# Kernel tuning notes

Measured on AMD Instinct MI355X. Metric: run time of the kernel, lower is better.

The kernel has to match this reference:

```python
import jax, jax.numpy as jnp
import numpy as np

B, T, C, H, D = 2, 2048, 1024, 16, 64


def setup_inputs() -> dict:
    key = jax.random.key(0)
    k1, k2, k3, k4, k5 = jax.random.split(key, 5)
    x = jax.random.normal(k1, (B, T, C), dtype=jnp.float32)
    Wq = jax.random.normal(k2, (H, C, D), dtype=jnp.float32) * 0.02
    Wk = jax.random.normal(k3, (H, C, D), dtype=jnp.float32) * 0.02
    Wv = jax.random.normal(k4, (H, C, D), dtype=jnp.float32) * 0.02
    Wo = jax.random.normal(k5, (C, C), dtype=jnp.float32) * 0.02
    bo = jnp.zeros((C,), dtype=jnp.float32)
    return {"x": x, "Wq": Wq, "Wk": Wk, "Wv": Wv, "Wo": Wo, "bo": bo}


def reference(x, Wq, Wk, Wv, Wo, bo):
    # per-head projections (batched over heads instead of a python loop)
    q = jnp.einsum('btc,hcd->bhtd', x, Wq)
    k = jnp.einsum('btc,hcd->bhtd', x, Wk)
    v = jnp.einsum('btc,hcd->bhtd', x, Wv)
    scale = jnp.asarray(D, x.dtype) ** -0.5
    wei = jnp.einsum('bhtd,bhsd->bhts', q, k) * scale  # [B,H,T,T]
    causal = jnp.tril(jnp.ones((T, T), dtype=bool))
    wei = jnp.where(causal, wei, jnp.asarray(-jnp.inf, wei.dtype))
    attn = jax.nn.softmax(wei, axis=-1)
    out = jnp.einsum('bhts,bhsd->bhtd', attn, v)  # [B,H,T,D]
    # concat heads (head order h0..hH-1 along feature dim)
    out = out.transpose(0, 2, 1, 3).reshape(B, T, C)
    # output projection: nn.Linear -> y = x @ W^T + b  (dropout p=0 is identity)
    return out @ Wo.T + bo
```

## Files before the change

### kernel.cpp

```cpp
#include <hip/hip_runtime.h>
#include <hip/hip_bf16.h>
#include <cstdint>
#include <math.h>

#define B_DIM 2
#define T_SEQ 2048
#define C_DIM 1024
#define H_NUM 16
#define D_HEAD 64
#define M_ROWS (B_DIM * T_SEQ)
#define N_QKV (3 * H_NUM * D_HEAD)

using short8  = __attribute__((ext_vector_type(8))) short;
using short4v = __attribute__((ext_vector_type(4))) short;
using f32x4   = __attribute__((ext_vector_type(4))) float;

__device__ __forceinline__ short f2bf(float f) {
  union { __hip_bfloat16 h; short s; } u;
  u.h = __float2bfloat16(f);
  return u.s;
}

__device__ __forceinline__ unsigned pk2bf(float a, float b) {
  union { float f; unsigned u; } ua, ub;
  ua.f = a; ub.f = b;
  return __builtin_amdgcn_perm(ub.u, ua.u, 0x07060302u);
}

__device__ __forceinline__ void gld_lds16(short* lds, const short* g) {
  __builtin_amdgcn_global_load_lds(
      (const unsigned int __attribute__((address_space(1)))*)g,
      (unsigned int __attribute__((address_space(3)))*)lds, 16, 0, 0);
}

#define BAR_VM(N)                                                    \
  do {                                                               \
    asm volatile("s_waitcnt vmcnt(" #N ") lgkmcnt(0)" ::: "memory"); \
    __builtin_amdgcn_s_barrier();                                    \
    __builtin_amdgcn_sched_barrier(0);                               \
  } while (0)

__global__ __launch_bounds__(256) void cvt_f32_bf16(const float* __restrict__ in,
                                                    short* __restrict__ out, int n8) {
  int i = blockIdx.x * 256 + threadIdx.x;
  if (i >= n8) return;
  const float4* p = reinterpret_cast<const float4*>(in) + (size_t)i * 2;
  float4 a = p[0], b = p[1];
  short8 o;
  o[0] = f2bf(a.x); o[1] = f2bf(a.y); o[2] = f2bf(a.z); o[3] = f2bf(a.w);
  o[4] = f2bf(b.x); o[5] = f2bf(b.y); o[6] = f2bf(b.z); o[7] = f2bf(b.w);
  reinterpret_cast<short8*>(out)[i] = o;
}

__global__ __launch_bounds__(256) void pack_w(const float* __restrict__ Wq,
                                              const float* __restrict__ Wk,
                                              const float* __restrict__ Wv,
                                              short* __restrict__ Wt) {
  int bid  = blockIdx.x;
  int proj = bid >> 8;
  int h    = (bid >> 4) & 15;
  int cb   = bid & 15;
  const float* W = (proj == 0) ? Wq : ((proj == 1) ? Wk : Wv);
  const float* src = W + ((size_t)h * C_DIM + (size_t)cb * 64) * D_HEAD;

  __shared__ float tile[64][65];
  int tid = threadIdx.x;

#pragma unroll
  for (int j = 0; j < 4; j++) {
    int flat = tid + j * 256;
    int c    = flat >> 4;
    int d4   = flat & 15;
    float4 v = reinterpret_cast<const float4*>(src + (size_t)c * D_HEAD)[d4];
    tile[c][d4 * 4 + 0] = v.x;
    tile[c][d4 * 4 + 1] = v.y;
    tile[c][d4 * 4 + 2] = v.z;
    tile[c][d4 * 4 + 3] = v.w;
  }
  __syncthreads();

  int d     = tid >> 2;
  int cpart = (tid & 3) * 16;
  short* dst = Wt + ((size_t)(proj * H_NUM + h) * D_HEAD + d) * C_DIM + cb * 64 + cpart;
  short8 o0, o1;
#pragma unroll
  for (int j = 0; j < 8; j++) {
    o0[j] = f2bf(tile[cpart + j][d]);
    o1[j] = f2bf(tile[cpart + 8 + j][d]);
  }
  *reinterpret_cast<short8*>(dst)     = o0;
  *reinterpret_cast<short8*>(dst + 8) = o1;
}

template <int MODE, int BMT>
__global__ __launch_bounds__(256) void gemm_bt(
    const short* __restrict__ A, const short* __restrict__ Bt,
    const float* __restrict__ bias,
    short* __restrict__ qb, short* __restrict__ kb, short* __restrict__ vtb,
    float* __restrict__ outb,
    int M, int N, int K) {
  constexpr int BK = 32;
  constexpr int MR = BMT / 32;
  constexpr int NLA = BMT / 64;
  __shared__ short GL[3 * (BMT + 128) * BK];
  short* Asb = GL;
  short* Bsb = GL + 3 * BMT * BK;

  int tid  = threadIdx.x;
  int lane = tid & 63;
  int wv   = tid >> 6;
  int q15  = lane & 15, g = lane >> 4;
  int ntn  = N >> 7;
  int bpx  = (M / BMT) >> 3;
  int xcd  = blockIdx.x & 7;
  int idx  = blockIdx.x >> 3;
  int bn   = idx / bpx;
  int bm   = xcd * bpx + (idx - bn * bpx);
  int row0 = bm * BMT, col0 = bn << 7;
  int wm   = (wv >> 1) * (BMT / 2);
  int wn   = (wv & 1) << 6;

  f32x4 acc[MR][4];
#pragma unroll
  for (int i = 0; i < MR; i++)
#pragma unroll
    for (int j = 0; j < 4; j++) acc[i][j] = (f32x4){0.f, 0.f, 0.f, 0.f};

  const short* ag = A  + (size_t)(row0 + (tid >> 2)) * K + (tid & 3) * 8;
  const short* bg = Bt + (size_t)(col0 + (tid >> 2)) * K + (tid & 3) * 8;
  const size_t gstep = (size_t)64 * K;

  auto stage = [&](int ks, int buf) {
    const short* a  = ag + (size_t)ks * BK;
    const short* bb = bg + (size_t)ks * BK;
    gld_lds16(Asb + buf * BMT * BK + tid * 8, a);
    if constexpr (NLA == 2)
      gld_lds16(Asb + buf * BMT * BK + 64 * BK + tid * 8, a + gstep);
    gld_lds16(Bsb + buf * 128 * BK + tid * 8, bb);
    gld_lds16(Bsb + buf * 128 * BK + 64 * BK + tid * 8, bb + gstep);
  };

  int nk = K / BK;
  stage(0, 0);
  stage(1, 1);
  if constexpr (NLA == 2) {
    asm volatile("s_waitcnt vmcnt(4)" ::: "memory");
  } else {
    asm volatile("s_waitcnt vmcnt(3)" ::: "memory");
  }
  __builtin_amdgcn_s_barrier();
  __builtin_amdgcn_sched_barrier(0);

  for (int k = 0; k < nk; ++k) {
    int buf = k % 3;
    if (k + 2 < nk) stage(k + 2, (k + 2) % 3);

    short8 af[MR], bf[4];
#pragma unroll
    for (int mi = 0; mi < MR; mi++)
      af[mi] = *reinterpret_cast<const short8*>(
          &Asb[buf * BMT * BK + (wm + mi * 16 + q15) * BK + g * 8]);
#pragma unroll
    for (int ni = 0; ni < 4; ni++)
      bf[ni] = *reinterpret_cast<const short8*>(
          &Bsb[buf * 128 * BK + (wn + ni * 16 + q15) * BK + g * 8]);
    __builtin_amdgcn_s_setprio(1);
#pragma unroll
    for (int mi = 0; mi < MR; mi++)
#pragma unroll
      for (int ni = 0; ni < 4; ni++)
        acc[mi][ni] = __builtin_amdgcn_mfma_f32_16x16x32_bf16(af[mi], bf[ni],
                                                              acc[mi][ni], 0, 0, 0);
    __builtin_amdgcn_s_setprio(0);

    if (k + 1 < nk) {
      if (k + 2 < nk) {
        if constexpr (NLA == 2) { BAR_VM(4); } else { BAR_VM(3); }
      } else {
        BAR_VM(0);
      }
    }
  }

  if constexpr (MODE == 0) {
    constexpr int LDT = 136;
    int proj  = col0 >> 10;
    int b     = row0 >> 11;
    int trow0 = row0 & (T_SEQ - 1);
    int h0    = (col0 >> 6) & 15;
    __syncthreads();
    if (proj < 2) {
      float scl = (proj == 0) ? 0.125f * 1.44269504f : 1.0f;
#pragma unroll
      for (int mi = 0; mi < MR; mi++)
#pragma unroll
        for (int ni = 0; ni < 4; ni++) {
          int t0 = wm + mi * 16 + (g << 2);
          int d2 = wn + ni * 16 + q15;
#pragma unroll
          for (int r = 0; r < 4; r++)
            GL[(t0 + r) * LDT + d2] = f2bf(acc[mi][ni][r] * scl);
        }
      __syncthreads();
      short* dstb = (proj == 0) ? qb : kb;
#pragma unroll
      for (int ps = 0; ps < 8; ps++) {
        int trow  = ps * 16 + (tid >> 4);
        int chunk = tid & 15;
        int hh    = h0 + (chunk >> 3);
        int d     = (chunk & 7) * 8;
        short8 v = *reinterpret_cast<const short8*>(&GL[trow * LDT + chunk * 8]);
        *reinterpret_cast<short8*>(
            dstb + ((size_t)(b * H_NUM + hh) * T_SEQ + trow0 + trow) * D_HEAD + d) = v;
      }
    } else {
#pragma unroll
      for (int mi = 0; mi < MR; mi++)
#pragma unroll
        for (int ni = 0; ni < 4; ni++) {
          int t0 = wm + mi * 16 + (g << 2);
          int d2 = wn + ni * 16 + q15;
          short4v pk;
#pragma unroll
          for (int r = 0; r < 4; r++) pk[r] = f2bf(acc[mi][ni][r]);
          *reinterpret_cast<short4v*>(&GL[d2 * LDT + t0]) = pk;
        }
      __syncthreads();
#pragma unroll
      for (int ps = 0; ps < 8; ps++) {
        int drow  = ps * 16 + (tid >> 4);
        int chunk = tid & 15;
        int hh    = h0 + (drow >> 6);
        int d     = drow & 63;
        short8 v = *reinterpret_cast<const short8*>(&GL[drow * LDT + chunk * 8]);
        *reinterpret_cast<short8*>(
            vtb + ((size_t)(b * H_NUM + hh) * D_HEAD + d) * T_SEQ + trow0 +
            chunk * 8) = v;
      }
    }
  } else {
#pragma unroll
    for (int mi = 0; mi < MR; mi++) {
#pragma unroll
      for (int ni = 0; ni < 4; ni++) {
        int rb  = row0 + wm + mi * 16 + (g << 2);
        int col = col0 + wn + ni * 16 + q15;
        f32x4 v = acc[mi][ni];
        float bb = bias[col];
#pragma unroll
        for (int r = 0; r < 4; r++)
          outb[(size_t)(rb + r) * N + col] = v[r] + bb;
      }
    }
  }
}

__global__ __launch_bounds__(256, 4) void attn_fwd(const short* __restrict__ qg,
                                                   const short* __restrict__ kg,
                                                   const short* __restrict__ vt,
                                                   short* __restrict__ ob) {
  int bid  = blockIdx.x;
  int q2   = bid >> 8;
  int r    = bid & 255;
  int bh   = (r & 7) * 4 + q2;
  int sb   = r >> 3;
  int strip = (q2 & 1) ? sb : 31 - sb;
  int b    = bh >> 4;
  int h    = bh & 15;
  int tid  = threadIdx.x, lane = tid & 63, wv = tid >> 6;
  int q15  = lane & 15, g = lane >> 4;
  int qr   = strip * 64 + wv * 16;

  __shared__ short arena[16384];

  const short* qp = qg + (size_t)bh * T_SEQ * D_HEAD;
  const short* kp = kg + (size_t)bh * T_SEQ * D_HEAD;
  const short* vp = vt + (size_t)bh * D_HEAD * T_SEQ;

  int r8    = lane >> 3;
  int gcb   = ((lane & 7) * 16) ^ (r8 << 4);
  int srow0 = wv * 16;

  int hh = (q15 & 7) << 4;
  int koff0 = ((0 * 64 + g * 16) ^ hh) >> 1;
  int koff1 = ((1 * 64 + g * 16) ^ hh) >> 1;
  int voff[4];
#pragma unroll
  for (int st = 0; st < 4; st++) voff[st] = ((st * 32 + g * 8) ^ hh) >> 1;

  short8 qf[2];
#pragma unroll
  for (int kk = 0; kk < 2; kk++)
    qf[kk] = *reinterpret_cast<const short8*>(
        qp + (size_t)(qr + q15) * D_HEAD + kk * 32 + g * 8);

  f32x4 acc[4];
#pragma unroll
  for (int dt = 0; dt < 4; dt++) acc[dt] = (f32x4){0.f, 0.f, 0.f, 0.f};
  f32x4 lacc = (f32x4){0.f, 0.f, 0.f, 0.f};
  float m_ = -1e30f;

  const short4v ones4 = (short4v){(short)0x3F80, (short)0x3F80,
                                  (short)0x3F80, (short)0x3F80};

  int nch = strip + 1;

  auto stage = [&](int c, int pbuf) {
    const short* ks = kp + (size_t)(c * 64 + srow0 + r8) * D_HEAD + (gcb >> 1);
    const short* vs = vp + (size_t)(srow0 + r8) * T_SEQ + c * 64 + (gcb >> 1);
    short* kd = arena + pbuf * 4096 + srow0 * 64 + lane * 8;
    short* vd = arena + 8192 + pbuf * 4096 + srow0 * 64 + lane * 8;
    gld_lds16(kd, ks);
    gld_lds16(kd + 8 * 64, ks + (size_t)8 * D_HEAD);
    gld_lds16(vd, vs);
    gld_lds16(vd + 8 * 64, vs + (size_t)8 * T_SEQ);
  };

  stage(0, 0);
  BAR_VM(0);

  for (int c = 0; c < nch; ++c) {
    int s0 = c * 64;
    if (c + 1 < nch) stage(c + 1, (c + 1) & 1);
    const short* Kb = arena + (c & 1) * 4096;
    const short* Vb = arena + 8192 + (c & 1) * 4096;

    short8 kf[4][2];
#pragma unroll
    for (int st = 0; st < 4; st++) {
      int rbase = (st * 16 + q15) * 64;
      kf[st][0] = *reinterpret_cast<const short8*>(&Kb[rbase + koff0]);
      kf[st][1] = *reinterpret_cast<const short8*>(&Kb[rbase + koff1]);
    }

    f32x4 sv[4];
    __builtin_amdgcn_s_setprio(1);
#pragma unroll
    for (int st = 0; st < 4; st++) {
      f32x4 s = (f32x4){0.f, 0.f, 0.f, 0.f};
      s = __builtin_amdgcn_mfma_f32_16x16x32_bf16(kf[st][0], qf[0], s, 0, 0, 0);
      s = __builtin_amdgcn_mfma_f32_16x16x32_bf16(kf[st][1], qf[1], s, 0, 0, 0);
      sv[st] = s;
    }
    __builtin_amdgcn_s_setprio(0);

    short4v vf[4][4];
#pragma unroll
    for (int st = 0; st < 4; st++)
#pragma unroll
      for (int dt = 0; dt < 4; dt++)
        vf[st][dt] = *reinterpret_cast<const short4v*>(
            &Vb[(dt * 16 + q15) * 64 + voff[st]]);

    if (c == nch - 1) {
#pragma unroll
      for (int st = 0; st < 4; st++)
#pragma unroll
        for (int r2 = 0; r2 < 4; r2++) {
          int sg = s0 + st * 16 + g * 4 + r2;
          if (sg > qr + q15) sv[st][r2] = -1e30f;
        }
    }

    float t0 = fmaxf(fmaxf(sv[0][0], sv[0][1]), sv[0][2]);
    float t1 = fmaxf(fmaxf(sv[0][3], sv[1][0]), sv[1][1]);
    float t2 = fmaxf(fmaxf(sv[1][2], sv[1][3]), sv[2][0]);
    float t3 = fmaxf(fmaxf(sv[2][1], sv[2][2]), sv[2][3]);
    float t4 = fmaxf(fmaxf(sv[3][0], sv[3][1]), sv[3][2]);
    float mx = fmaxf(fmaxf(fmaxf(t0, t1), t2),
                     fmaxf(fmaxf(t3, t4), sv[3][3]));
    mx = fmaxf(mx, __shfl_xor(mx, 16));
    mx = fmaxf(mx, __shfl_xor(mx, 32));

    if (!__all(mx <= m_ + 11.5f)) {
      float mnew = fmaxf(m_, mx);
      float sc   = __builtin_amdgcn_exp2f(m_ - mnew);
      m_ = mnew;
      lacc *= sc;
#pragma unroll
      for (int dt = 0; dt < 4; dt++) acc[dt] *= sc;
    }
    float mcur = m_;

    short4v pbf[4];
#pragma unroll
    for (int st = 0; st < 4; st++) {
      float p0 = __builtin_amdgcn_exp2f(sv[st][0] - mcur);
      float p1 = __builtin_amdgcn_exp2f(sv[st][1] - mcur);
      float p2 = __builtin_amdgcn_exp2f(sv[st][2] - mcur);
      float p3 = __builtin_amdgcn_exp2f(sv[st][3] - mcur);
      union { short4v s; unsigned u[2]; } P;
      P.u[0] = pk2bf(p0, p1);
      P.u[1] = pk2bf(p2, p3);
      pbf[st] = P.s;
    }

    __builtin_amdgcn_s_setprio(1);
#pragma unroll
    for (int st = 0; st < 4; st++) {
#if __has_builtin(__builtin_amdgcn_mfma_f32_16x16x16bf16_1k)
      lacc = __builtin_amdgcn_mfma_f32_16x16x16bf16_1k(ones4, pbf[st], lacc, 0, 0, 0);
#pragma unroll
      for (int dt = 0; dt < 4; dt++)
        acc[dt] = __builtin_amdgcn_mfma_f32_16x16x16bf16_1k(
            vf[st][dt], pbf[st], acc[dt], 0, 0, 0);
#else
      short4v p4 = pbf[st];
      short8 bz = (short8){p4[0], p4[1], p4[2], p4[3], 0, 0, 0, 0};
      short8 oz = (short8){(short)0x3F80, (short)0x3F80, (short)0x3F80,
                           (short)0x3F80, 0, 0, 0, 0};
      lacc = __builtin_amdgcn_mfma_f32_16x16x32_bf16(oz, bz, lacc, 0, 0, 0);
#pragma unroll
      for (int dt = 0; dt < 4; dt++) {
        short4v v4 = vf[st][dt];
        short8 az = (short8){v4[0], v4[1], v4[2], v4[3], 0, 0, 0, 0};
        acc[dt] =
            __builtin_amdgcn_mfma_f32_16x16x32_bf16(az, bz, acc[dt], 0, 0, 0);
      }
#endif
    }
    __builtin_amdgcn_s_setprio(0);

    BAR_VM(0);
  }

  short* OlW = arena + wv * (16 * 68);
  float inv = 1.0f / lacc[0];
#pragma unroll
  for (int dt = 0; dt < 4; dt++)
#pragma unroll
    for (int r2 = 0; r2 < 4; r2++)
      OlW[q15 * 68 + dt * 16 + g * 4 + r2] = f2bf(acc[dt][r2] * inv);
  int row = lane >> 2, cb = (lane & 3) * 16;
  size_t base = ((size_t)(b * T_SEQ) + qr + row) * C_DIM + h * 64 + cb;
  const short* src = OlW + row * 68 + cb;
  *reinterpret_cast<short8*>(ob + base) = *reinterpret_cast<const short8*>(src);
  *reinterpret_cast<short8*>(ob + base + 8) =
      *reinterpret_cast<const short8*>(src + 8);
}

extern "C" void kernel_launch(void* const* d_in, const int* in_sizes, int n_in,
                              void* d_out, int out_size, void* d_ws, size_t ws_size,
                              hipStream_t stream) {
  const float* x  = (const float*)d_in[0];
  const float* Wq = (const float*)d_in[1];
  const float* Wk = (const float*)d_in[2];
  const float* Wv = (const float*)d_in[3];
  const float* Wo = (const float*)d_in[4];
  const float* bo = (const float*)d_in[5];
  float* out = (float*)d_out;

  char* ws = (char*)d_ws;
  short* xb   = (short*)(ws + 0);
  short* Wt   = (short*)(ws + 8388608);
  short* Wob  = (short*)(ws + 14680064);
  short* qb   = (short*)(ws + 16777216);
  short* kb   = (short*)(ws + 25165824);
  short* vtb  = (short*)(ws + 33554432);
  short* obuf = xb;

  cvt_f32_bf16<<<2048, 256, 0, stream>>>(x, xb, M_ROWS * C_DIM / 8);
  cvt_f32_bf16<<<512, 256, 0, stream>>>(Wo, Wob, C_DIM * C_DIM / 8);
  pack_w<<<768, 256, 0, stream>>>(Wq, Wk, Wv, Wt);

  gemm_bt<0, 128><<<(M_ROWS / 128) * (N_QKV / 128), 256, 0, stream>>>(
      xb, Wt, nullptr, qb, kb, vtb, nullptr, M_ROWS, N_QKV, C_DIM);

  attn_fwd<<<1024, 256, 0, stream>>>(qb, kb, vtb, obuf);

  gemm_bt<1, 64><<<(M_ROWS / 64) * (C_DIM / 128), 256, 0, stream>>>(
      obuf, Wob, bo, nullptr, nullptr, nullptr, out, M_ROWS, C_DIM, C_DIM);
}
```

Measured before the change: 110.1 us.

## Software-pipeline LDS fragment loads against MFMA in the GEMM main loop

Restructures the GEMM k-loop so the LDS reads for the next k-step go into a second set of register fragments while MFMAs run on the current set. The loop is unrolled by two with ping-pong fragment buffers, and the prologue and epilogue are adjusted to match. The aim is to hide LDS read latency behind matrix-core work instead of stalling before each MFMA block. In exchange it doubles fragment register usage, which could lower occupancy, and the barrier and staging ordering across the triple-buffered LDS becomes more intricate.

```diff
diff --git a/kernel.cpp b/kernel.cpp
--- a/kernel.cpp
+++ b/kernel.cpp
@@ -140,7 +140,32 @@
     gld_lds16(Bsb + buf * 128 * BK + 64 * BK + tid * 8, bb + gstep);
   };
 
+  auto readf = [&](int ks, short8 (&af)[MR], short8 (&bf)[4]) {
+    int buf = ks % 3;
+#pragma unroll
+    for (int mi = 0; mi < MR; mi++)
+      af[mi] = *reinterpret_cast<const short8*>(
+          &Asb[buf * BMT * BK + (wm + mi * 16 + q15) * BK + g * 8]);
+#pragma unroll
+    for (int ni = 0; ni < 4; ni++)
+      bf[ni] = *reinterpret_cast<const short8*>(
+          &Bsb[buf * 128 * BK + (wn + ni * 16 + q15) * BK + g * 8]);
+  };
+
+  auto domfma = [&](short8 (&af)[MR], short8 (&bf)[4]) {
+    __builtin_amdgcn_s_setprio(1);
+#pragma unroll
+    for (int mi = 0; mi < MR; mi++)
+#pragma unroll
+      for (int ni = 0; ni < 4; ni++)
+        acc[mi][ni] = __builtin_amdgcn_mfma_f32_16x16x32_bf16(af[mi], bf[ni],
+                                                              acc[mi][ni], 0, 0, 0);
+    __builtin_amdgcn_s_setprio(0);
+  };
+
   int nk = K / BK;
+  short8 fa0[MR], fb0[4], fa1[MR], fb1[4];
+
   stage(0, 0);
   stage(1, 1);
   if constexpr (NLA == 2) {
@@ -151,35 +176,39 @@
   __builtin_amdgcn_s_barrier();
   __builtin_amdgcn_sched_barrier(0);
 
-  for (int k = 0; k < nk; ++k) {
-    int buf = k % 3;
+  readf(0, fa0, fb0);
+  if (nk > 2) stage(2, 2);
+  if (nk > 2) {
+    if constexpr (NLA == 2) { BAR_VM(4); } else { BAR_VM(3); }
+  } else {
+    BAR_VM(0);
+  }
+
+  int k = 1;
+  for (; k + 1 < nk; k += 2) {
+    readf(k, fa1, fb1);
     if (k + 2 < nk) stage(k + 2, (k + 2) % 3);
-
-    short8 af[MR], bf[4];
-#pragma unroll
-    for (int mi = 0; mi < MR; mi++)
-      af[mi] = *reinterpret_cast<const short8*>(
-          &Asb[buf * BMT * BK + (wm + mi * 16 + q15) * BK + g * 8]);
-#pragma unroll
-    for (int ni = 0; ni < 4; ni++)
-      bf[ni] = *reinterpret_cast<const short8*>(
-          &Bsb[buf * 128 * BK + (wn + ni * 16 + q15) * BK + g * 8]);
-    __builtin_amdgcn_s_setprio(1);
-#pragma unroll
-    for (int mi = 0; mi < MR; mi++)
-#pragma unroll
-      for (int ni = 0; ni < 4; ni++)
-        acc[mi][ni] = __builtin_amdgcn_mfma_f32_16x16x32_bf16(af[mi], bf[ni],
-                                                              acc[mi][ni], 0, 0, 0);
-    __builtin_amdgcn_s_setprio(0);
-
-    if (k + 1 < nk) {
-      if (k + 2 < nk) {
-        if constexpr (NLA == 2) { BAR_VM(4); } else { BAR_VM(3); }
-      } else {
-        BAR_VM(0);
-      }
-    }
+    domfma(fa0, fb0);
+    if (k + 2 < nk) {
+      if constexpr (NLA == 2) { BAR_VM(4); } else { BAR_VM(3); }
+    } else {
+      BAR_VM(0);
+    }
+    readf(k + 1, fa0, fb0);
+    if (k + 3 < nk) stage(k + 3, (k + 3) % 3);
+    domfma(fa1, fb1);
+    if (k + 3 < nk) {
+      if constexpr (NLA == 2) { BAR_VM(4); } else { BAR_VM(3); }
+    } else {
+      BAR_VM(0);
+    }
+  }
+  if (k < nk) {
+    readf(k, fa1, fb1);
+    domfma(fa0, fb0);
+    domfma(fa1, fb1);
+  } else {
+    domfma(fa0, fb0);
   }
 
   if constexpr (MODE == 0) {
```

Result: no change. 108.4 us (-1.5%).
